# Kernel optimization log

Hardware: AMD Instinct MI355X
Metric: run time of the kernel (lower is better)

The kernel has to match this reference:

```python
import jax, jax.numpy as jnp
import numpy as np

N_NODES = 100000
N_EDGES = 1200000
N_GRAPHS = 128
IN_C, HID_C, OUT_C = 64, 128, 16


def setup_inputs() -> dict:
    key = jax.random.key(0)
    ks = jax.random.split(key, 6)
    x = jax.random.normal(ks[0], (N_NODES, IN_C), dtype=jnp.float32)
    edge_index = jax.random.randint(ks[1], (2, N_EDGES), 0, N_NODES, dtype=jnp.int64)
    batch = jnp.sort(jax.random.randint(ks[2], (N_NODES,), 0, N_GRAPHS, dtype=jnp.int64))
    W1 = jax.random.normal(ks[3], (IN_C, HID_C), dtype=jnp.float32) * (1.0 / np.sqrt(IN_C))
    b1 = jnp.zeros((HID_C,), jnp.float32)
    W2 = jax.random.normal(ks[4], (HID_C, OUT_C), dtype=jnp.float32) * (1.0 / np.sqrt(HID_C))
    b2 = jnp.zeros((OUT_C,), jnp.float32)
    return {"x": x, "edge_index": edge_index, "batch": batch,
            "W1": W1, "b1": b1, "W2": W2, "b2": b2}


def gcn_conv(x, src, dst, W, b, n):
    """PyG GCNConv: add self-loops, symmetric deg^{-1/2} normalization, scatter-add."""
    h = x @ W                                   # [n, out] dense transform first
    loop = jnp.arange(n, dtype=src.dtype)
    s = jnp.concatenate([src, loop])            # edges + self-loops
    d = jnp.concatenate([dst, loop])
    deg = jax.ops.segment_sum(jnp.ones(d.shape[0], h.dtype), d, num_segments=n)
    dinv = jnp.where(deg > 0, jax.lax.rsqrt(deg), jnp.zeros((), h.dtype))
    norm = dinv[s] * dinv[d]                    # [E + n]
    msg = h[s] * norm[:, None]                  # gather + scale
    return jax.ops.segment_sum(msg, d, num_segments=n) + b  # scatter-add


def reference(x, edge_index, batch, W1, b1, W2, b2):
    n = x.shape[0]
    src, dst = edge_index[0], edge_index[1]
    h = jax.nn.relu(gcn_conv(x, src, dst, W1, b1, n))
    h = gcn_conv(h, src, dst, W2, b2, n)
    # global_mean_pool over batch ids
    sums = jax.ops.segment_sum(h, batch, num_segments=N_GRAPHS)
    cnts = jax.ops.segment_sum(jnp.ones((n,), h.dtype), batch, num_segments=N_GRAPHS)
    pooled = sums / jnp.maximum(cnts, 1.0)[:, None]   # [N_GRAPHS, OUT_C]
    return jax.nn.log_softmax(pooled, axis=1)
```

## Files before the change

### kernel.cpp

```cpp
#include <hip/hip_runtime.h>
#include <hip/hip_bf16.h>


#define THREADS 256
#define NPB 256
#define BSTRIDE 4096
#define CH 4096
#define NBMAX 512
#define NGRAPH 128

typedef __attribute__((ext_vector_type(8))) short bf16x8;
typedef __attribute__((ext_vector_type(4))) float f32x4;

__device__ __forceinline__ float bfu_lo(unsigned int u) {
    union { unsigned int i; float f; } v; v.i = u << 16; return v.f;
}
__device__ __forceinline__ float bfu_hi(unsigned int u) {
    union { unsigned int i; float f; } v; v.i = u & 0xffff0000u; return v.f;
}
__device__ __forceinline__ unsigned short f2bf(float f) {
    union { float f; unsigned int i; } v; v.f = f;
    unsigned int r = v.i + 0x7fff + ((v.i >> 16) & 1);
    return (unsigned short)(r >> 16);
}
__device__ __forceinline__ unsigned int packbf(float lo, float hi) {
    return (unsigned int)f2bf(lo) | ((unsigned int)f2bf(hi) << 16);
}
__device__ __forceinline__ void unpack8(uint4 u, float* f) {
    f[0] = bfu_lo(u.x); f[1] = bfu_hi(u.x);
    f[2] = bfu_lo(u.y); f[3] = bfu_hi(u.y);
    f[4] = bfu_lo(u.z); f[5] = bfu_hi(u.z);
    f[6] = bfu_lo(u.w); f[7] = bfu_hi(u.w);
}
__device__ __forceinline__ void unpack4(uint2 u, float* f) {
    f[0] = bfu_lo(u.x); f[1] = bfu_hi(u.x);
    f[2] = bfu_lo(u.y); f[3] = bfu_hi(u.y);
}

__global__ __launch_bounds__(THREADS) void k_partition(const int* __restrict__ src,
                                                       const int* __restrict__ dst,
                                                       int* __restrict__ bucketCursor,
                                                       unsigned int* __restrict__ ebuf,
                                                       int E, int NB) {
    __shared__ int h[NBMAX];
    __shared__ int base[NBMAX];
    __shared__ int cnt[NBMAX];
    __shared__ int dL[CH];
    for (int b = threadIdx.x; b < NBMAX; b += THREADS) { h[b] = 0; cnt[b] = 0; }
    __syncthreads();
    int b0 = blockIdx.x * CH;
    for (int k = 0; k < CH; k += THREADS) {
        int e = b0 + k + threadIdx.x;
        if (e < E) {
            int d = dst[e];
            dL[k + threadIdx.x] = d;
            atomicAdd(&h[d >> 8], 1);
        }
    }
    __syncthreads();
    for (int b = threadIdx.x; b < NB; b += THREADS)
        if (h[b]) base[b] = b * BSTRIDE + atomicAdd(&bucketCursor[b], h[b]);
    __syncthreads();
    for (int k = 0; k < CH; k += THREADS) {
        int e = b0 + k + threadIdx.x;
        if (e < E) {
            int s = src[e];
            int d = dL[k + threadIdx.x];
            int b = d >> 8;
            int i = base[b] + atomicAdd(&cnt[b], 1);
            ebuf[i] = ((unsigned int)(d & (NPB - 1)) << 17) | (unsigned int)s;
        }
    }
}

__global__ __launch_bounds__(THREADS) void k_bucket_csr(const unsigned int* __restrict__ ebuf,
                                                        const int* __restrict__ bucketCursor,
                                                        const float* __restrict__ x,
                                                        int* __restrict__ offs,
                                                        int* __restrict__ deg,
                                                        int* __restrict__ srcs,
                                                        float* __restrict__ dinv,
                                                        uint4* __restrict__ xnb,
                                                        int n) {
    __shared__ unsigned int eL[BSTRIDE];
    __shared__ int c[NPB];
    __shared__ int cur[NPB];
    __shared__ float dloc[NPB];
    __shared__ int sh[THREADS];
    const int tid = threadIdx.x;
    const int b = blockIdx.x;
    const int nbase = b * NPB;
    const int w0 = b * BSTRIDE;
    const int cnt_b = bucketCursor[b];
    c[tid] = 0;
    __syncthreads();
    for (int i = tid; i < cnt_b; i += THREADS) {
        unsigned int e = ebuf[w0 + i];
        eL[i] = e;
        atomicAdd(&c[e >> 17], 1);
    }
    __syncthreads();
    int c0 = c[tid];
    sh[tid] = c0;
    __syncthreads();
    for (int step = 1; step < THREADS; step <<= 1) {
        int t = (tid >= step) ? sh[tid - step] : 0;
        __syncthreads();
        sh[tid] += t;
        __syncthreads();
    }
    int excl = sh[tid] - c0;
    int node = nbase + tid;
    float dv = rsqrtf((float)(c0 + 1));
    dloc[tid] = dv;
    if (node < n) {
        offs[node] = w0 + excl;
        deg[node] = c0;
        dinv[node] = dv;
    }
    cur[tid] = excl;
    __syncthreads();
    for (int i = tid; i < cnt_b; i += THREADS) {
        unsigned int e = eL[i];
        int pos = w0 + atomicAdd(&cur[e >> 17], 1);
        srcs[pos] = (int)(e & 0x1FFFFu);
    }
    const float4* X4 = (const float4*)x;
    for (int i = tid; i < NPB * 8; i += THREADS) {
        int ln = i >> 3;
        int node2 = nbase + ln;
        if (node2 >= n) break;
        int q = i & 7;
        float dd = dloc[ln];
        float4 a = X4[(size_t)node2 * 16 + q * 2];
        float4 bb = X4[(size_t)node2 * 16 + q * 2 + 1];
        uint4 o;
        o.x = packbf(a.x * dd, a.y * dd);
        o.y = packbf(a.z * dd, a.w * dd);
        o.z = packbf(bb.x * dd, bb.y * dd);
        o.w = packbf(bb.z * dd, bb.w * dd);
        xnb[(size_t)node2 * 8 + q] = o;
    }
}

__global__ __launch_bounds__(THREADS) void k_gather1(const int* __restrict__ offs,
                                                     const int* __restrict__ deg,
                                                     const int* __restrict__ srcs,
                                                     const float* __restrict__ dinv,
                                                     const uint4* __restrict__ xnb,
                                                     uint4* __restrict__ aggb, int n) {
    int idx = blockIdx.x * THREADS + threadIdx.x;
    int node = idx >> 3;
    if (node >= n) return;
    int q = idx & 7;
    float acc[8];
    unpack8(xnb[(size_t)node * 8 + q], acc);
    int e0 = offs[node], e1 = e0 + deg[node];
    int e = e0;
    for (; e + 1 < e1; e += 2) {
        int s0 = srcs[e], s1 = srcs[e + 1];
        float t0[8], t1[8];
        unpack8(xnb[(size_t)s0 * 8 + q], t0);
        unpack8(xnb[(size_t)s1 * 8 + q], t1);
#pragma unroll
        for (int j = 0; j < 8; ++j) acc[j] += t0[j] + t1[j];
    }
    if (e < e1) {
        int s = srcs[e];
        float t[8];
        unpack8(xnb[(size_t)s * 8 + q], t);
#pragma unroll
        for (int j = 0; j < 8; ++j) acc[j] += t[j];
    }
    float dd = dinv[node];
    uint4 o;
    o.x = packbf(acc[0] * dd, acc[1] * dd);
    o.y = packbf(acc[2] * dd, acc[3] * dd);
    o.z = packbf(acc[4] * dd, acc[5] * dd);
    o.w = packbf(acc[6] * dd, acc[7] * dd);
    aggb[(size_t)node * 8 + q] = o;
}

__global__ __launch_bounds__(THREADS) void k_gemm12m(const unsigned short* __restrict__ aggb,
                                                     const float* __restrict__ W1,
                                                     const float* __restrict__ b1,
                                                     const float* __restrict__ W2,
                                                     const float* __restrict__ dinv,
                                                     unsigned short* __restrict__ ts,
                                                     int n, int ntiles) {
    __shared__ unsigned short h1L[4][16][136];
    const int wave = threadIdx.x >> 6;
    const int lane = threadIdx.x & 63;
    const int col = lane & 15;
    const int ko = lane >> 4;

    bf16x8 bfr1[2][8];
#pragma unroll
    for (int ks = 0; ks < 2; ++ks)
#pragma unroll
        for (int nt = 0; nt < 8; ++nt) {
            bf16x8 b;
#pragma unroll
            for (int j = 0; j < 8; ++j)
                b[j] = (short)f2bf(W1[(ks * 32 + ko * 8 + j) * 128 + nt * 16 + col]);
            bfr1[ks][nt] = b;
        }
    float bias[8];
#pragma unroll
    for (int nt = 0; nt < 8; ++nt) bias[nt] = b1[nt * 16 + col];
    bf16x8 bfr2[4];
#pragma unroll
    for (int ks = 0; ks < 4; ++ks) {
        bf16x8 b;
#pragma unroll
        for (int j = 0; j < 8; ++j)
            b[j] = (short)f2bf(W2[(ks * 32 + ko * 8 + j) * 16 + col]);
        bfr2[ks] = b;
    }

    const int tile0 = (blockIdx.x * 4 + wave) * 4;
    for (int t = 0; t < 4; ++t) {
        int tile = tile0 + t;
        if (tile >= ntiles) return;
        int r0 = tile * 16;
        int rowA = r0 + col;
        if (rowA >= n) rowA = n - 1;
        const bf16x8* Ap = (const bf16x8*)(aggb + (size_t)rowA * 64 + ko * 8);
        bf16x8 a0 = Ap[0];
        bf16x8 a1 = Ap[4];
        f32x4 acc[8];
#pragma unroll
        for (int nt = 0; nt < 8; ++nt) acc[nt] = (f32x4){0.f, 0.f, 0.f, 0.f};
#pragma unroll
        for (int nt = 0; nt < 8; ++nt) {
            acc[nt] = __builtin_amdgcn_mfma_f32_16x16x32_bf16(a0, bfr1[0][nt], acc[nt], 0, 0, 0);
            acc[nt] = __builtin_amdgcn_mfma_f32_16x16x32_bf16(a1, bfr1[1][nt], acc[nt], 0, 0, 0);
        }
#pragma unroll
        for (int nt = 0; nt < 8; ++nt)
#pragma unroll
            for (int r = 0; r < 4; ++r)
                h1L[wave][ko * 4 + r][nt * 16 + col] = f2bf(fmaxf(acc[nt][r] + bias[nt], 0.f));
        f32x4 acc2 = (f32x4){0.f, 0.f, 0.f, 0.f};
#pragma unroll
        for (int ks = 0; ks < 4; ++ks) {
            bf16x8 a2 = *(const bf16x8*)&h1L[wave][col][ks * 32 + ko * 8];
            acc2 = __builtin_amdgcn_mfma_f32_16x16x32_bf16(a2, bfr2[ks], acc2, 0, 0, 0);
        }
#pragma unroll
        for (int r = 0; r < 4; ++r) {
            int row = r0 + ko * 4 + r;
            if (row < n) {
                float dd = dinv[row];
                ts[(size_t)row * 16 + col] = f2bf(acc2[r] * dd);
            }
        }
    }
}

__global__ __launch_bounds__(THREADS) void k_gatherpool(const int* __restrict__ offs,
                                                        const int* __restrict__ deg,
                                                        const int* __restrict__ srcs,
                                                        const float* __restrict__ dinv,
                                                        const uint2* __restrict__ ts,
                                                        const int* __restrict__ batch,
                                                        float* __restrict__ sums, int n) {
    __shared__ float gsum[8 * 16];
    __shared__ int gminS;
    const int tid = threadIdx.x;
    if (tid < 128) gsum[tid] = 0.f;
    if (tid == 0) {
        int first = min((blockIdx.x * THREADS) >> 2, n - 1);
        gminS = batch[first];
    }
    __syncthreads();
    const int gmin = gminS;
    int idx = blockIdx.x * THREADS + tid;
    int node = idx >> 2;
    if (node < n) {
        int q = idx & 3;
        float acc[4];
        unpack4(ts[(size_t)node * 4 + q], acc);
        int e0 = offs[node], e1 = e0 + deg[node];
        int e = e0;
        for (; e + 1 < e1; e += 2) {
            int s0 = srcs[e], s1 = srcs[e + 1];
            float t0[4], t1[4];
            unpack4(ts[(size_t)s0 * 4 + q], t0);
            unpack4(ts[(size_t)s1 * 4 + q], t1);
#pragma unroll
            for (int j = 0; j < 4; ++j) acc[j] += t0[j] + t1[j];
        }
        if (e < e1) {
            int s = srcs[e];
            float t[4];
            unpack4(ts[(size_t)s * 4 + q], t);
#pragma unroll
            for (int j = 0; j < 4; ++j) acc[j] += t[j];
        }
        float dd = dinv[node];
        int g = batch[node];
        int local = g - gmin;
        if ((unsigned)local < 8u) {
            float* row = &gsum[local * 16 + q * 4];
#pragma unroll
            for (int j = 0; j < 4; ++j) atomicAdd(&row[j], acc[j] * dd);
        } else {
            float* row = &sums[g * 16 + q * 4];
#pragma unroll
            for (int j = 0; j < 4; ++j) atomicAdd(&row[j], acc[j] * dd);
        }
    }
    __syncthreads();
    if (tid < 128) {
        float v = gsum[tid];
        int g = gmin + (tid >> 4);
        if (v != 0.f && g < NGRAPH) atomicAdd(&sums[g * 16 + (tid & 15)], v);
    }
}

__global__ __launch_bounds__(NGRAPH) void k_final(const float* __restrict__ sums,
                                                  const int* __restrict__ batch,
                                                  const float* __restrict__ b2,
                                                  float* __restrict__ out, int n) {
    int g = threadIdx.x;
    int lo = 0, hi = n;
    while (lo < hi) { int mid = (lo + hi) >> 1; if (batch[mid] < g) lo = mid + 1; else hi = mid; }
    int s0 = lo;
    hi = n;
    while (lo < hi) { int mid = (lo + hi) >> 1; if (batch[mid] < g + 1) lo = mid + 1; else hi = mid; }
    int s1 = lo;
    float cnt = fmaxf((float)(s1 - s0), 1.0f);
    float v[16];
    float mx = -1e30f;
#pragma unroll
    for (int c = 0; c < 16; ++c) {
        v[c] = sums[g * 16 + c] / cnt + b2[c];
        mx = fmaxf(mx, v[c]);
    }
    float se = 0.f;
#pragma unroll
    for (int c = 0; c < 16; ++c) se += expf(v[c] - mx);
    float lse = logf(se) + mx;
#pragma unroll
    for (int c = 0; c < 16; ++c) out[g * 16 + c] = v[c] - lse;
}

extern "C" void kernel_launch(void* const* d_in, const int* in_sizes, int n_in,
                              void* d_out, int out_size, void* d_ws, size_t ws_size,
                              hipStream_t stream) {
    const float* x    = (const float*)d_in[0];
    const int* edges  = (const int*)d_in[1];
    const int* batch  = (const int*)d_in[2];
    const float* W1   = (const float*)d_in[3];
    const float* b1   = (const float*)d_in[4];
    const float* W2   = (const float*)d_in[5];
    const float* b2   = (const float*)d_in[6];
    float* out        = (float*)d_out;

    const int n = in_sizes[2];
    const int E = in_sizes[1] / 2;
    const int* src = edges;
    const int* dst = edges + E;
    const int NB = (n + NPB - 1) / NPB;
    const int npart = (E + CH - 1) / CH;
    const int ntiles = (n + 15) / 16;

    char* ws = (char*)d_ws;
    size_t off = 0;
    auto carve = [&](size_t bytes) { char* p = ws + off; off = (off + bytes + 255) & ~(size_t)255; return p; };
    int*   bucketCursor = (int*)carve(NBMAX * 4);
    float* sums    = (float*)carve(NGRAPH * 16 * 4);
    int*   offs    = (int*)carve((size_t)n * 4);
    int*   deg     = (int*)carve((size_t)n * 4);
    int*   srcs    = (int*)carve((size_t)NB * BSTRIDE * 4);
    float* dinv    = (float*)carve((size_t)n * 4);
    uint4* xnb     = (uint4*)carve((size_t)n * 64 * 2);
    char*  aggreg  = (char*)carve((size_t)n * 64 * 2);
    char*  big     = (char*)carve((size_t)NB * BSTRIDE * 4 > (size_t)n * 128 * 2
                                  ? (size_t)NB * BSTRIDE * 4 : (size_t)n * 128 * 2);
    unsigned int* ebuf = (unsigned int*)big;
    unsigned short* ts = (unsigned short*)big;
    unsigned short* aggb = (unsigned short*)aggreg;

    auto blks = [](long long work) { return (int)((work + THREADS - 1) / THREADS); };

    hipMemsetAsync(bucketCursor, 0, NBMAX * 4 + NGRAPH * 16 * 4, stream);
    k_partition  <<<npart, THREADS, 0, stream>>>(src, dst, bucketCursor, ebuf, E, NB);
    k_bucket_csr <<<NB, THREADS, 0, stream>>>(ebuf, bucketCursor, x, offs, deg, srcs, dinv, xnb, n);

    k_gather1 <<<blks((long long)n * 8), THREADS, 0, stream>>>(offs, deg, srcs, dinv, xnb, (uint4*)aggb, n);
    k_gemm12m <<<(ntiles + 15) / 16, THREADS, 0, stream>>>(aggb, W1, b1, W2, dinv, ts, n, ntiles);

    k_gatherpool <<<blks((long long)n * 4), THREADS, 0, stream>>>(offs, deg, srcs, dinv,
                                                                  (const uint2*)ts, batch, sums, n);
    k_final <<<1, NGRAPH, 0, stream>>>(sums, batch, b2, out, n);
}
```

Before: 118.5 us.

## Split normalized features into column-quarter planes for cache-local gather

The bf16 scaled feature array is stored as four planes of 16 columns each (32 bytes per node per plane) instead of one interleaved row. The first-layer gather launches four blocks per 64-node group, each handling one quarter plane, with 4 lanes per node reading 8 bytes each. The aim is a smaller random-access working set per plane so gathered rows stay cache-resident, and edge indices are read with nontemporal loads. In exchange the neighbor index list and degree are read four times, and each gathered access is narrower.

```diff
diff --git a/kernel.cpp b/kernel.cpp
--- a/kernel.cpp
+++ b/kernel.cpp
@@ -80,7 +80,7 @@
                                                         int* __restrict__ deg,
                                                         int* __restrict__ srcs,
                                                         float* __restrict__ dinv,
-                                                        uint4* __restrict__ xnb,
+                                                        uint4* __restrict__ xnbP4,
                                                         int n) {
     __shared__ unsigned int eL[BSTRIDE];
     __shared__ int c[NPB];
@@ -139,7 +139,7 @@
         o.y = packbf(a.z * dd, a.w * dd);
         o.z = packbf(bb.x * dd, bb.y * dd);
         o.w = packbf(bb.z * dd, bb.w * dd);
-        xnb[(size_t)node2 * 8 + q] = o;
+        xnbP4[(size_t)(q >> 1) * n * 2 + (size_t)node2 * 2 + (q & 1)] = o;
     }
 }
 
@@ -147,38 +147,38 @@
                                                      const int* __restrict__ deg,
                                                      const int* __restrict__ srcs,
                                                      const float* __restrict__ dinv,
-                                                     const uint4* __restrict__ xnb,
-                                                     uint4* __restrict__ aggb, int n) {
-    int idx = blockIdx.x * THREADS + threadIdx.x;
-    int node = idx >> 3;
+                                                     const uint2* __restrict__ xnbP,
+                                                     unsigned short* __restrict__ aggb, int n) {
+    const int quarter = blockIdx.x & 3;
+    const int node = (blockIdx.x >> 2) * 64 + (threadIdx.x >> 2);
     if (node >= n) return;
-    int q = idx & 7;
-    float acc[8];
-    unpack8(xnb[(size_t)node * 8 + q], acc);
+    const int sub = threadIdx.x & 3;
+    const uint2* plane = xnbP + (size_t)quarter * n * 4;
+    float acc[4];
+    unpack4(plane[(size_t)node * 4 + sub], acc);
     int e0 = offs[node], e1 = e0 + deg[node];
     int e = e0;
     for (; e + 1 < e1; e += 2) {
-        int s0 = srcs[e], s1 = srcs[e + 1];
-        float t0[8], t1[8];
-        unpack8(xnb[(size_t)s0 * 8 + q], t0);
-        unpack8(xnb[(size_t)s1 * 8 + q], t1);
-#pragma unroll
-        for (int j = 0; j < 8; ++j) acc[j] += t0[j] + t1[j];
+        int s0 = __builtin_nontemporal_load(srcs + e);
+        int s1 = __builtin_nontemporal_load(srcs + e + 1);
+        float t0[4], t1[4];
+        unpack4(plane[(size_t)s0 * 4 + sub], t0);
+        unpack4(plane[(size_t)s1 * 4 + sub], t1);
+#pragma unroll
+        for (int j = 0; j < 4; ++j) acc[j] += t0[j] + t1[j];
     }
     if (e < e1) {
-        int s = srcs[e];
-        float t[8];
-        unpack8(xnb[(size_t)s * 8 + q], t);
-#pragma unroll
-        for (int j = 0; j < 8; ++j) acc[j] += t[j];
+        int s = __builtin_nontemporal_load(srcs + e);
+        float t[4];
+        unpack4(plane[(size_t)s * 4 + sub], t);
+#pragma unroll
+        for (int j = 0; j < 4; ++j) acc[j] += t[j];
     }
     float dd = dinv[node];
-    uint4 o;
+    uint2 o;
     o.x = packbf(acc[0] * dd, acc[1] * dd);
     o.y = packbf(acc[2] * dd, acc[3] * dd);
-    o.z = packbf(acc[4] * dd, acc[5] * dd);
-    o.w = packbf(acc[6] * dd, acc[7] * dd);
-    aggb[(size_t)node * 8 + q] = o;
+    *(uint2*)(aggb + (size_t)node * 64 + quarter * 16 + sub * 4) = o;
 }
 
 __global__ __launch_bounds__(THREADS) void k_gemm12m(const unsigned short* __restrict__ aggb,
@@ -375,7 +375,7 @@
     int*   deg     = (int*)carve((size_t)n * 4);
     int*   srcs    = (int*)carve((size_t)NB * BSTRIDE * 4);
     float* dinv    = (float*)carve((size_t)n * 4);
-    uint4* xnb     = (uint4*)carve((size_t)n * 64 * 2);
+    uint4* xnbP4   = (uint4*)carve((size_t)n * 64 * 2);
     char*  aggreg  = (char*)carve((size_t)n * 64 * 2);
     char*  big     = (char*)carve((size_t)NB * BSTRIDE * 4 > (size_t)n * 128 * 2
                                   ? (size_t)NB * BSTRIDE * 4 : (size_t)n * 128 * 2);
@@ -387,9 +387,11 @@
 
     hipMemsetAsync(bucketCursor, 0, NBMAX * 4 + NGRAPH * 16 * 4, stream);
     k_partition  <<<npart, THREADS, 0, stream>>>(src, dst, bucketCursor, ebuf, E, NB);
-    k_bucket_csr <<<NB, THREADS, 0, stream>>>(ebuf, bucketCursor, x, offs, deg, srcs, dinv, xnb, n);
-
-    k_gather1 <<<blks((long long)n * 8), THREADS, 0, stream>>>(offs, deg, srcs, dinv, xnb, (uint4*)aggb, n);
+    k_bucket_csr <<<NB, THREADS, 0, stream>>>(ebuf, bucketCursor, x, offs, deg, srcs, dinv, xnbP4, n);
+
+    const int nblkn = (n + 63) / 64;
+    k_gather1 <<<nblkn * 4, THREADS, 0, stream>>>(offs, deg, srcs, dinv,
+                                                  (const uint2*)xnbP4, aggb, n);
     k_gemm12m <<<(ntiles + 15) / 16, THREADS, 0, stream>>>(aggb, W1, b1, W2, dinv, ts, n, ntiles);
 
     k_gatherpool <<<blks((long long)n * 4), THREADS, 0, stream>>>(offs, deg, srcs, dinv,
```

Result: slower. 161.2 us (+36.1%).
